# Optimization experiments

Hardware: AMD Instinct MI355X
Metric: run time of the kernel (lower is better)

The kernel has to match this reference:

```python
import jax, jax.numpy as jnp
import numpy as np

T = 1.0  # temperature (init kwarg t)
N, M, D = 16384, 16384, 64


def setup_inputs() -> dict:
    key = jax.random.key(0)
    k1, k2, k3 = jax.random.split(key, 3)
    logits = jax.random.normal(k1, (N, D), dtype=jnp.float32)
    targets = jax.random.normal(k2, (M, D), dtype=jnp.float32)
    # probabilities in (0,1]; bounded away from 0 so log is finite
    noise_probs = jax.random.uniform(k3, (D,), dtype=jnp.float32, minval=1e-3, maxval=1.0)
    return {"logits": logits, "targets": targets, "noise_probs": noise_probs}


def reference(logits, targets, noise_probs):
    # q: (N, d) = logits / t - log(noise_probs)
    q = logits / T - jnp.log(noise_probs)[None, :]
    # The torch repeat/unsqueeze/reshape broadcast-multiply-sum is exactly a GEMM:
    # scores[n, m] = sum_d q[n, d] * targets[m, d]
    scores = jnp.einsum('nd,md->nm', q, targets)  # (N, M)
    # subtract detached row max (numerical stabilization, no grad through max)
    scores = scores - jax.lax.stop_gradient(jnp.max(scores, axis=1, keepdims=True))
    # CrossEntropyLoss with labels = arange(N) (non-distributed path), mean reduction
    logp = jax.nn.log_softmax(scores, axis=1)  # (N, M)
    labels = jnp.arange(scores.shape[0])
    picked = jnp.take_along_axis(logp, labels[:, None], axis=1)[:, 0]  # (N,)
    return -jnp.mean(picked)
```

## Files before the change

### kernel.cpp

```cpp
#include <hip/hip_runtime.h>
#include <hip/hip_bf16.h>
#include <stdint.h>

#define N_ROWS 16384
#define D_DIM 64
#define BN 128
#define BM 128
#define NSPLIT 8
#define COLS_PER_SPLIT (N_ROWS / NSPLIT)
#define N_ITER (COLS_PER_SPLIT / BM)
#define SHIFT2 64.0f
#define LOG2E 1.44269504088896340736f
#define LN2 0.69314718055994530942f

using short8  = __attribute__((ext_vector_type(8))) short;
using float4v = __attribute__((ext_vector_type(4))) float;

__device__ __forceinline__ unsigned short f2bf(float f) {
  unsigned u = __float_as_uint(f);
  unsigned r = (u + 0x7fffu + ((u >> 16) & 1u)) >> 16;
  return (unsigned short)r;
}
__device__ __forceinline__ float blo(unsigned u) { return __uint_as_float(u << 16); }
__device__ __forceinline__ float bhi(unsigned u) { return __uint_as_float(u & 0xffff0000u); }

__device__ __forceinline__ void async_stage_16(const void* g, void* l) {
  __builtin_amdgcn_global_load_lds(
      (const __attribute__((address_space(1))) uint32_t*)g,
      (__attribute__((address_space(3))) uint32_t*)l, 16, 0, 0);
}

__device__ __forceinline__ void stage_tile(const uint8_t* gbase, uint8_t* lds,
                                           int wave, int lane) {
#pragma unroll
  for (int q = 0; q < 4; ++q) {
    int t = wave * 4 + q;
    int row = t * 8 + (lane >> 3);
    int c = (lane & 7) ^ (row & 7);
    async_stage_16(gbase + row * 128 + c * 16, lds + t * 1024 + lane * 16);
  }
}

__global__ void prep_kernel(const float4* __restrict__ lg,
                            const float4* __restrict__ tg,
                            const float* __restrict__ noise,
                            ushort4* __restrict__ qa,
                            ushort4* __restrict__ tb,
                            float* __restrict__ row_sums,
                            float* __restrict__ out) {
  int i = blockIdx.x * blockDim.x + threadIdx.x;
  if (i < N_ROWS) row_sums[i] = 0.f;
  if (i == 0) out[0] = 0.f;
  int d4 = (i & 15) << 2;
  float4 l = lg[i];
  float4 t = tg[i];
  float c0 = log2f(noise[d4 + 0]);
  float c1 = log2f(noise[d4 + 1]);
  float c2 = log2f(noise[d4 + 2]);
  float c3 = log2f(noise[d4 + 3]);
  ushort4 ua, ub;
  ua.x = f2bf(l.x * LOG2E - c0);
  ua.y = f2bf(l.y * LOG2E - c1);
  ua.z = f2bf(l.z * LOG2E - c2);
  ua.w = f2bf(l.w * LOG2E - c3);
  ub.x = f2bf(t.x);
  ub.y = f2bf(t.y);
  ub.z = f2bf(t.z);
  ub.w = f2bf(t.w);
  qa[i] = ua;
  tb[i] = ub;
}

__global__ __launch_bounds__(256, 2) void flash_kernel(
    const uint8_t* __restrict__ qa,
    const uint8_t* __restrict__ tb,
    float* __restrict__ row_sums) {
  __shared__ __align__(16) uint8_t ldsA[BN * 128];
  __shared__ __align__(16) uint8_t ldsB[BM * 128];

  const int bid = blockIdx.x;
  const int rb = bid >> 3;
  const int sp = bid & 7;
  const int tid = threadIdx.x;
  const int wave = tid >> 6;
  const int lane = tid & 63;

  const int row0 = rb * BN;
  const int col0 = sp * COLS_PER_SPLIT;

  stage_tile(qa + (size_t)row0 * 128, ldsA, wave, lane);
  stage_tile(tb + (size_t)col0 * 128, ldsB, wave, lane);
  __syncthreads();

  const int rows_off = (wave >> 1) * 64;
  const int cols_off = (wave & 1) * 64;

  short8 afrag[4][2];
#pragma unroll
  for (int i = 0; i < 4; ++i)
#pragma unroll
    for (int k2 = 0; k2 < 2; ++k2) {
      int r = rows_off + i * 16 + (lane & 15);
      int c = (k2 * 4 + (lane >> 4)) ^ (r & 7);
      afrag[i][k2] = *(const short8*)(ldsA + r * 128 + c * 16);
    }

  float sums[4][4];
#pragma unroll
  for (int i = 0; i < 4; ++i)
#pragma unroll
    for (int r = 0; r < 4; ++r) sums[i][r] = 0.f;

  for (int it = 0; it < N_ITER; ++it) {
    short8 bfrag[4][2];
#pragma unroll
    for (int j = 0; j < 4; ++j)
#pragma unroll
      for (int k2 = 0; k2 < 2; ++k2) {
        int r = cols_off + j * 16 + (lane & 15);
        int c = (k2 * 4 + (lane >> 4)) ^ (r & 7);
        bfrag[j][k2] = *(const short8*)(ldsB + r * 128 + c * 16);
      }
    __syncthreads();
    if (it + 1 < N_ITER)
      stage_tile(tb + (size_t)(col0 + (it + 1) * BM) * 128, ldsB, wave, lane);

    float4v acc[4][4];
#pragma unroll
    for (int i = 0; i < 4; ++i)
#pragma unroll
      for (int j = 0; j < 4; ++j) {
        float4v a0 = {-SHIFT2, -SHIFT2, -SHIFT2, -SHIFT2};
        a0 = __builtin_amdgcn_mfma_f32_16x16x32_bf16(afrag[i][0], bfrag[j][0], a0, 0, 0, 0);
        a0 = __builtin_amdgcn_mfma_f32_16x16x32_bf16(afrag[i][1], bfrag[j][1], a0, 0, 0, 0);
        acc[i][j] = a0;
      }
#pragma unroll
    for (int i = 0; i < 4; ++i)
#pragma unroll
      for (int j = 0; j < 4; ++j)
#pragma unroll
        for (int r = 0; r < 4; ++r)
          sums[i][r] += __builtin_amdgcn_exp2f(acc[i][j][r]);
    __syncthreads();
  }

#pragma unroll
  for (int i = 0; i < 4; ++i)
#pragma unroll
    for (int r = 0; r < 4; ++r) {
      float v = sums[i][r];
      v += __shfl_xor(v, 1);
      v += __shfl_xor(v, 2);
      v += __shfl_xor(v, 4);
      v += __shfl_xor(v, 8);
      if ((lane & 15) == 0) {
        int grow = row0 + rows_off + i * 16 + (lane >> 4) * 4 + r;
        atomicAdd(&row_sums[grow], v);
      }
    }
}

__global__ void finish_kernel(const uint4* __restrict__ qa,
                              const uint4* __restrict__ tb,
                              const float* __restrict__ row_sums,
                              float* __restrict__ out) {
  int n = blockIdx.x * blockDim.x + threadIdx.x;
  const uint4* a = qa + n * 8;
  const uint4* b = tb + n * 8;
  float diag = 0.f;
#pragma unroll
  for (int c = 0; c < 8; ++c) {
    uint4 ua = a[c], ub = b[c];
    diag += blo(ua.x) * blo(ub.x) + bhi(ua.x) * bhi(ub.x);
    diag += blo(ua.y) * blo(ub.y) + bhi(ua.y) * bhi(ub.y);
    diag += blo(ua.z) * blo(ub.z) + bhi(ua.z) * bhi(ub.z);
    diag += blo(ua.w) * blo(ub.w) + bhi(ua.w) * bhi(ub.w);
  }
  float loss = LN2 * (SHIFT2 + log2f(row_sums[n]) - diag);
#pragma unroll
  for (int off = 32; off; off >>= 1) loss += __shfl_down(loss, off);
  if ((threadIdx.x & 63) == 0) atomicAdd(out, loss * (1.0f / N_ROWS));
}

extern "C" void kernel_launch(void* const* d_in, const int* in_sizes, int n_in,
                              void* d_out, int out_size, void* d_ws, size_t ws_size,
                              hipStream_t stream) {
  const float* logits  = (const float*)d_in[0];
  const float* targets = (const float*)d_in[1];
  const float* noise   = (const float*)d_in[2];
  float* out = (float*)d_out;

  uint8_t* ws = (uint8_t*)d_ws;
  uint8_t* qa = ws;
  uint8_t* tb = ws + (size_t)2 * 1024 * 1024;
  float* row_sums = (float*)(ws + (size_t)4 * 1024 * 1024);

  prep_kernel<<<1024, 256, 0, stream>>>(
      (const float4*)logits, (const float4*)targets, noise,
      (ushort4*)qa, (ushort4*)tb, row_sums, out);

  flash_kernel<<<NSPLIT * (N_ROWS / BN), 256, 0, stream>>>(qa, tb, row_sums);

  finish_kernel<<<N_ROWS / 256, 256, 0, stream>>>(
      (const uint4*)qa, (const uint4*)tb, row_sums, out);
}
```

Baseline: 111.0 us.

## Drop LDS staging; load MFMA fragments directly from global per wave

The flash kernel no longer stages tiles in LDS with async loads and barriers. Each wave independently owns 64 rows and 1/16 of the columns and reads its B fragments straight from global memory (through L2/L1). The diagonal dot product moves into the prep kernel so the finish kernel only reads row sums and the diagonal, and log(noise) is computed once per block in shared memory. This removes barrier synchronisation and LDS traffic but relies on cache hits for the heavily reused B matrix, with uncoalesced 16-byte fragment loads.

```diff
diff --git a/kernel.cpp b/kernel.cpp
--- a/kernel.cpp
+++ b/kernel.cpp
@@ -4,11 +4,9 @@
 
 #define N_ROWS 16384
 #define D_DIM 64
-#define BN 128
-#define BM 128
-#define NSPLIT 8
+#define NSPLIT 16
 #define COLS_PER_SPLIT (N_ROWS / NSPLIT)
-#define N_ITER (COLS_PER_SPLIT / BM)
+#define N_ITER (COLS_PER_SPLIT / 64)
 #define SHIFT2 64.0f
 #define LOG2E 1.44269504088896340736f
 #define LN2 0.69314718055994530942f
@@ -21,24 +19,8 @@
   unsigned r = (u + 0x7fffu + ((u >> 16) & 1u)) >> 16;
   return (unsigned short)r;
 }
-__device__ __forceinline__ float blo(unsigned u) { return __uint_as_float(u << 16); }
-__device__ __forceinline__ float bhi(unsigned u) { return __uint_as_float(u & 0xffff0000u); }
-
-__device__ __forceinline__ void async_stage_16(const void* g, void* l) {
-  __builtin_amdgcn_global_load_lds(
-      (const __attribute__((address_space(1))) uint32_t*)g,
-      (__attribute__((address_space(3))) uint32_t*)l, 16, 0, 0);
-}
-
-__device__ __forceinline__ void stage_tile(const uint8_t* gbase, uint8_t* lds,
-                                           int wave, int lane) {
-#pragma unroll
-  for (int q = 0; q < 4; ++q) {
-    int t = wave * 4 + q;
-    int row = t * 8 + (lane >> 3);
-    int c = (lane & 7) ^ (row & 7);
-    async_stage_16(gbase + row * 128 + c * 16, lds + t * 1024 + lane * 16);
-  }
+__device__ __forceinline__ float bf2f(unsigned short s) {
+  return __uint_as_float(((unsigned)s) << 16);
 }
 
 __global__ void prep_kernel(const float4* __restrict__ lg,
@@ -47,63 +29,62 @@
                             ushort4* __restrict__ qa,
                             ushort4* __restrict__ tb,
                             float* __restrict__ row_sums,
+                            float* __restrict__ diag,
                             float* __restrict__ out) {
-  int i = blockIdx.x * blockDim.x + threadIdx.x;
+  __shared__ float l2n[64];
+  int tid = threadIdx.x;
+  if (tid < 64) l2n[tid] = log2f(noise[tid]);
+  __syncthreads();
+
+  int i = blockIdx.x * blockDim.x + tid;
   if (i < N_ROWS) row_sums[i] = 0.f;
   if (i == 0) out[0] = 0.f;
+
   int d4 = (i & 15) << 2;
   float4 l = lg[i];
   float4 t = tg[i];
-  float c0 = log2f(noise[d4 + 0]);
-  float c1 = log2f(noise[d4 + 1]);
-  float c2 = log2f(noise[d4 + 2]);
-  float c3 = log2f(noise[d4 + 3]);
   ushort4 ua, ub;
-  ua.x = f2bf(l.x * LOG2E - c0);
-  ua.y = f2bf(l.y * LOG2E - c1);
-  ua.z = f2bf(l.z * LOG2E - c2);
-  ua.w = f2bf(l.w * LOG2E - c3);
+  ua.x = f2bf(l.x * LOG2E - l2n[d4 + 0]);
+  ua.y = f2bf(l.y * LOG2E - l2n[d4 + 1]);
+  ua.z = f2bf(l.z * LOG2E - l2n[d4 + 2]);
+  ua.w = f2bf(l.w * LOG2E - l2n[d4 + 3]);
   ub.x = f2bf(t.x);
   ub.y = f2bf(t.y);
   ub.z = f2bf(t.z);
   ub.w = f2bf(t.w);
   qa[i] = ua;
   tb[i] = ub;
+
+  float part = bf2f(ua.x) * bf2f(ub.x) + bf2f(ua.y) * bf2f(ub.y) +
+               bf2f(ua.z) * bf2f(ub.z) + bf2f(ua.w) * bf2f(ub.w);
+  part += __shfl_xor(part, 1);
+  part += __shfl_xor(part, 2);
+  part += __shfl_xor(part, 4);
+  part += __shfl_xor(part, 8);
+  if ((tid & 15) == 0) diag[i >> 4] = part;
 }
 
-__global__ __launch_bounds__(256, 2) void flash_kernel(
+__global__ __launch_bounds__(256, 4) void flash_kernel(
     const uint8_t* __restrict__ qa,
     const uint8_t* __restrict__ tb,
     float* __restrict__ row_sums) {
-  __shared__ __align__(16) uint8_t ldsA[BN * 128];
-  __shared__ __align__(16) uint8_t ldsB[BM * 128];
-
-  const int bid = blockIdx.x;
-  const int rb = bid >> 3;
-  const int sp = bid & 7;
-  const int tid = threadIdx.x;
-  const int wave = tid >> 6;
-  const int lane = tid & 63;
-
-  const int row0 = rb * BN;
+  const int lane = threadIdx.x & 63;
+  const int gwave = blockIdx.x * 4 + (threadIdx.x >> 6);
+  const int rg = gwave >> 4;
+  const int sp = gwave & 15;
+  const int row0 = rg * 64;
   const int col0 = sp * COLS_PER_SPLIT;
 
-  stage_tile(qa + (size_t)row0 * 128, ldsA, wave, lane);
-  stage_tile(tb + (size_t)col0 * 128, ldsB, wave, lane);
-  __syncthreads();
-
-  const int rows_off = (wave >> 1) * 64;
-  const int cols_off = (wave & 1) * 64;
+  const int m = lane & 15;
+  const int kc = lane >> 4;
 
   short8 afrag[4][2];
 #pragma unroll
   for (int i = 0; i < 4; ++i)
 #pragma unroll
-    for (int k2 = 0; k2 < 2; ++k2) {
-      int r = rows_off + i * 16 + (lane & 15);
-      int c = (k2 * 4 + (lane >> 4)) ^ (r & 7);
-      afrag[i][k2] = *(const short8*)(ldsA + r * 128 + c * 16);
-    }
+    for (int k2 = 0; k2 < 2; ++k2)
+      afrag[i][k2] = *(const short8*)(qa + (size_t)(row0 + i * 16 + m) * 128 +
+                                      (k2 * 4 + kc) * 16);
 
   float sums[4][4];
 #pragma unroll
@@ -111,38 +92,33 @@
 #pragma unroll
     for (int r = 0; r < 4; ++r) sums[i][r] = 0.f;
 
+  const uint8_t* bbase = tb + (size_t)(col0 + m) * 128 + kc * 16;
+
+#pragma unroll 2
   for (int it = 0; it < N_ITER; ++it) {
     short8 bfrag[4][2];
 #pragma unroll
     for (int j = 0; j < 4; ++j)
 #pragma unroll
-      for (int k2 = 0; k2 < 2; ++k2) {
-        int r = cols_off + j * 16 + (lane & 15);
-        int c = (k2 * 4 + (lane >> 4)) ^ (r & 7);
-        bfrag[j][k2] = *(const short8*)(ldsB + r * 128 + c * 16);
-      }
-    __syncthreads();
-    if (it + 1 < N_ITER)
-      stage_tile(tb + (size_t)(col0 + (it + 1) * BM) * 128, ldsB, wave, lane);
+      for (int k2 = 0; k2 < 2; ++k2)
+        bfrag[j][k2] = *(const short8*)(bbase + it * 8192 + j * 2048 + k2 * 64);
 
-    float4v acc[4][4];
 #pragma unroll
-    for (int i = 0; i < 4; ++i)
+    for (int j = 0; j < 4; ++j) {
+      float4v acc[4];
 #pragma unroll
-      for (int j = 0; j < 4; ++j) {
+      for (int i = 0; i < 4; ++i) {
         float4v a0 = {-SHIFT2, -SHIFT2, -SHIFT2, -SHIFT2};
         a0 = __builtin_amdgcn_mfma_f32_16x16x32_bf16(afrag[i][0], bfrag[j][0], a0, 0, 0, 0);
         a0 = __builtin_amdgcn_mfma_f32_16x16x32_bf16(afrag[i][1], bfrag[j][1], a0, 0, 0, 0);
-        acc[i][j] = a0;
+        acc[i] = a0;
       }
 #pragma unroll
-    for (int i = 0; i < 4; ++i)
-#pragma unroll
-      for (int j = 0; j < 4; ++j)
+      for (int i = 0; i < 4; ++i)
 #pragma unroll
         for (int r = 0; r < 4; ++r)
-          sums[i][r] += __builtin_amdgcn_exp2f(acc[i][j][r]);
-    __syncthreads();
+          sums[i][r] += __builtin_amdgcn_exp2f(acc[i][r]);
+    }
   }
 
 #pragma unroll
@@ -154,30 +130,18 @@
       v += __shfl_xor(v, 2);
       v += __shfl_xor(v, 4);
       v += __shfl_xor(v, 8);
-      if ((lane & 15) == 0) {
-        int grow = row0 + rows_off + i * 16 + (lane >> 4) * 4 + r;
+      if (m == 0) {
+        int grow = row0 + i * 16 + kc * 4 + r;
         atomicAdd(&row_sums[grow], v);
       }
     }
 }
 
-__global__ void finish_kernel(const uint4* __restrict__ qa,
-                              const uint4* __restrict__ tb,
-                              const float* __restrict__ row_sums,
+__global__ void finish_kernel(const float* __restrict__ row_sums,
+                              const float* __restrict__ diag,
                               float* __restrict__ out) {
   int n = blockIdx.x * blockDim.x + threadIdx.x;
-  const uint4* a = qa + n * 8;
-  const uint4* b = tb + n * 8;
-  float diag = 0.f;
-#pragma unroll
-  for (int c = 0; c < 8; ++c) {
-    uint4 ua = a[c], ub = b[c];
-    diag += blo(ua.x) * blo(ub.x) + bhi(ua.x) * bhi(ub.x);
-    diag += blo(ua.y) * blo(ub.y) + bhi(ua.y) * bhi(ub.y);
-    diag += blo(ua.z) * blo(ub.z) + bhi(ua.z) * bhi(ub.z);
-    diag += blo(ua.w) * blo(ub.w) + bhi(ua.w) * bhi(ub.w);
-  }
-  float loss = LN2 * (SHIFT2 + log2f(row_sums[n]) - diag);
+  float loss = LN2 * (SHIFT2 + log2f(row_sums[n]) - diag[n]);
 #pragma unroll
   for (int off = 32; off; off >>= 1) loss += __shfl_down(loss, off);
   if ((threadIdx.x & 63) == 0) atomicAdd(out, loss * (1.0f / N_ROWS));
@@ -195,13 +159,13 @@
   uint8_t* qa = ws;
   uint8_t* tb = ws + (size_t)2 * 1024 * 1024;
   float* row_sums = (float*)(ws + (size_t)4 * 1024 * 1024);
+  float* diag     = (float*)(ws + (size_t)4 * 1024 * 1024 + 65536);
 
   prep_kernel<<<1024, 256, 0, stream>>>(
       (const float4*)logits, (const float4*)targets, noise,
-      (ushort4*)qa, (ushort4*)tb, row_sums, out);
+      (ushort4*)qa, (ushort4*)tb, row_sums, diag, out);
 
-  flash_kernel<<<NSPLIT * (N_ROWS / BN), 256, 0, stream>>>(qa, tb, row_sums);
+  flash_kernel<<<(256 * NSPLIT) / 4, 256, 0, stream>>>(qa, tb, row_sums);
 
-  finish_kernel<<<N_ROWS / 256, 256, 0, stream>>>(
-      (const uint4*)qa, (const uint4*)tb, row_sums, out);
+  finish_kernel<<<N_ROWS / 256, 256, 0, stream>>>(row_sums, diag, out);
 }
```

Result: slower. 134.1 us (+20.7%).
